# Kernel tuning notes

Measured on AMD Instinct MI355X. Metric: run time of the kernel, lower is better.

## Reference

```python
import jax, jax.numpy as jnp
import numpy as np

N_WIRES = 5
N_OPS = 100000
BATCH = 64
TWO_PI = 6.283185307179586


def _apply_1q(state, U, axis):
    # Apply a shared 2x2 unitary U to the given wire axis of state [B,2,2,2,2,2].
    s = jnp.moveaxis(state, axis, -1)
    s = jnp.einsum('ij,...j->...i', U, s)
    return jnp.moveaxis(s, -1, axis)


def _apply_1q_batched(state, U, axis):
    # Per-batch 2x2 unitaries U: [B,2,2].
    s = jnp.moveaxis(state, axis, -1)
    s = jnp.einsum('bij,b...j->b...i', U, s)
    return jnp.moveaxis(s, -1, axis)


def _rot_unitaries(angles, types):
    # Build [n_ops,2,2] complex64 unitaries: type 0 -> RX, 1 -> RY, 2 -> RZ.
    half = angles * 0.5
    c = jnp.cos(half).astype(jnp.complex64)
    s = jnp.sin(half).astype(jnp.complex64)
    mis = (-1j) * s
    Urx = jnp.stack([jnp.stack([c, mis], -1), jnp.stack([mis, c], -1)], -2)
    Ury = jnp.stack([jnp.stack([c, -s], -1), jnp.stack([s, c], -1)], -2)
    e = jnp.exp((-1j) * half)  # complex64
    zero = jnp.zeros_like(e)
    Urz = jnp.stack([jnp.stack([e, zero], -1), jnp.stack([zero, jnp.conj(e)], -1)], -2)
    t = types[:, None, None]
    return jnp.where(t == 0, Urx, jnp.where(t == 1, Ury, Urz))


def _forward(x, gate_angles, gate_wires, gate_types):
    B = x.shape[0]
    # |00000> initial state per batch item
    state = jnp.zeros((B,) + (2,) * N_WIRES, jnp.complex64)
    state = state.at[(slice(None),) + (0,) * N_WIRES].set(1.0)

    # RxEncoder: RX(x[:, k]) on wire k
    half = x * 0.5
    c = jnp.cos(half).astype(jnp.complex64)
    s = jnp.sin(half).astype(jnp.complex64)
    for k in range(N_WIRES):
        U = jnp.stack([jnp.stack([c[:, k], (-1j) * s[:, k]], -1),
                       jnp.stack([(-1j) * s[:, k], c[:, k]], -1)], -2)  # [B,2,2]
        state = _apply_1q_batched(state, U, k + 1)

    # RandomLayer: long sequential chain of tiny gates on a resident state vector
    Us = _rot_unitaries(gate_angles, gate_types)
    branches = [lambda st, U, a=k + 1: _apply_1q(st, U, a) for k in range(N_WIRES)]

    def step(st, inp):
        U, w = inp
        return jax.lax.switch(w, branches, st, U), None

    state, _ = jax.lax.scan(step, state, (Us, gate_wires))

    # Measure: expval of PauliY on every wire -> [B, 5]
    Y = jnp.array([[0.0, -1j], [1j, 0.0]], jnp.complex64)
    outs = []
    for k in range(N_WIRES):
        ys = _apply_1q(state, Y, k + 1)
        outs.append(jnp.sum(jnp.conj(state) * ys, axis=tuple(range(1, N_WIRES + 1))).real)
    return jnp.stack(outs, -1)


def setup_inputs() -> dict:
    key = jax.random.key(0)
    k1, k2, k3, k4 = jax.random.split(key, 4)
    x = jax.random.normal(k1, (BATCH, N_WIRES), dtype=jnp.float32)
    gate_angles = jax.random.uniform(k2, (N_OPS,), dtype=jnp.float32) * TWO_PI
    gate_wires = jax.random.randint(k3, (N_OPS,), 0, N_WIRES, dtype=jnp.int32)
    gate_types = jax.random.randint(k4, (N_OPS,), 0, 3, dtype=jnp.int32)
    return {"x": x, "gate_angles": gate_angles, "gate_wires": gate_wires, "gate_types": gate_types}


def reference(x, gate_angles, gate_wires, gate_types):
    return _forward(x, gate_angles, gate_wires, gate_types)
```

## Files before the change

### kernel.cpp

```cpp
#include <hip/hip_runtime.h>


#define N_WIRES 5
#define BATCH 64
#define BLOCKS_A 64
#define THREADS_A 256
#define LANES (BLOCKS_A * THREADS_A)
#define QTUP (N_WIRES * 4)

__device__ __forceinline__ void qmul(float* r, const float* b, const float* a) {
    r[0] = b[0]*a[0] - b[1]*a[1] - b[2]*a[2] - b[3]*a[3];
    r[1] = b[0]*a[1] + b[1]*a[0] + b[2]*a[3] - b[3]*a[2];
    r[2] = b[0]*a[2] - b[1]*a[3] + b[2]*a[0] + b[3]*a[1];
    r[3] = b[0]*a[3] + b[1]*a[2] - b[2]*a[1] + b[3]*a[0];
}

__device__ __forceinline__ void wave_reduce6(float* t) {
    for (int st = 1; st < 64; st <<= 1) {
        float o[QTUP];
        #pragma unroll
        for (int i = 0; i < QTUP; ++i) o[i] = __shfl_down(t[i], st, 64);
        #pragma unroll
        for (int w = 0; w < N_WIRES; ++w) {
            float r[4];
            qmul(r, &o[4*w], &t[4*w]);
            t[4*w+0] = r[0]; t[4*w+1] = r[1]; t[4*w+2] = r[2]; t[4*w+3] = r[3];
        }
    }
}

__global__ __launch_bounds__(THREADS_A)
void gate_partials(const float* __restrict__ angles,
                   const int*   __restrict__ wires,
                   const int*   __restrict__ types,
                   int n_ops, int chunk,
                   float* __restrict__ ws)
{
    const int lane = blockIdx.x * THREADS_A + threadIdx.x;

    float acc[N_WIRES][4];
    #pragma unroll
    for (int w = 0; w < N_WIRES; ++w) {
        acc[w][0] = 1.f; acc[w][1] = 0.f; acc[w][2] = 0.f; acc[w][3] = 0.f;
    }

    const int g0 = lane * chunk;
    const int g1 = min(g0 + chunk, n_ops);
    for (int g = g0; g < g1; ++g) {
        const float ang = angles[g];
        const int   w   = wires[g];
        const int   t   = types[g];
        float s, c;
        __sincosf(0.5f * ang, &s, &c);

        float qw = acc[0][0], qx = acc[0][1], qy = acc[0][2], qz = acc[0][3];
        #pragma unroll
        for (int k = 1; k < N_WIRES; ++k) {
            const bool m = (w == k);
            qw = m ? acc[k][0] : qw;  qx = m ? acc[k][1] : qx;
            qy = m ? acc[k][2] : qy;  qz = m ? acc[k][3] : qz;
        }
        const float pw = (t == 0) ? -qx : (t == 1) ? -qy : -qz;
        const float px = (t == 0) ?  qw : (t == 1) ?  qz : -qy;
        const float py = (t == 0) ? -qz : (t == 1) ?  qw :  qx;
        const float pz = (t == 0) ?  qy : (t == 1) ? -qx :  qw;
        const float nw = c*qw + s*pw;
        const float nx = c*qx + s*px;
        const float ny = c*qy + s*py;
        const float nz = c*qz + s*pz;
        #pragma unroll
        for (int k = 0; k < N_WIRES; ++k) {
            const bool m = (w == k);
            acc[k][0] = m ? nw : acc[k][0];  acc[k][1] = m ? nx : acc[k][1];
            acc[k][2] = m ? ny : acc[k][2];  acc[k][3] = m ? nz : acc[k][3];
        }
    }

    float t[QTUP];
    #pragma unroll
    for (int i = 0; i < QTUP; ++i) t[i] = acc[i >> 2][i & 3];
    wave_reduce6(t);

    __shared__ float lds[4][QTUP];
    const int wave = threadIdx.x >> 6;
    if ((threadIdx.x & 63) == 0) {
        #pragma unroll
        for (int i = 0; i < QTUP; ++i) lds[wave][i] = t[i];
    }
    __syncthreads();
    if (threadIdx.x == 0) {
        float r[QTUP];
        #pragma unroll
        for (int i = 0; i < QTUP; ++i) r[i] = lds[0][i];
        #pragma unroll
        for (int v = 1; v < 4; ++v) {
            #pragma unroll
            for (int w = 0; w < N_WIRES; ++w) {
                float z[4];
                qmul(z, &lds[v][4*w], &r[4*w]);
                r[4*w+0] = z[0]; r[4*w+1] = z[1]; r[4*w+2] = z[2]; r[4*w+3] = z[3];
            }
        }
        #pragma unroll
        for (int i = 0; i < QTUP; ++i) ws[blockIdx.x * QTUP + i] = r[i];
    }
}

__global__ __launch_bounds__(320)
void finalize(const float* __restrict__ x,
              const float* __restrict__ ws,
              float* __restrict__ out)
{
    __shared__ float U[QTUP];
    const int tid = threadIdx.x;
    if (tid < 64) {
        float t[QTUP];
        #pragma unroll
        for (int i = 0; i < QTUP; ++i) t[i] = ws[tid * QTUP + i];
        wave_reduce6(t);
        if (tid == 0) {
            #pragma unroll
            for (int i = 0; i < QTUP; ++i) U[i] = t[i];
        }
    }
    __syncthreads();

    if (tid < BATCH * N_WIRES) {
        const int b = tid / N_WIRES;
        const int k = tid % N_WIRES;
        const float xv = x[b * N_WIRES + k];
        float sx, cx;
        __sincosf(0.5f * xv, &sx, &cx);
        const float* q = &U[4*k];
        const float v0r =  cx*q[0] - sx*q[1];
        const float v0i = -cx*q[3] + sx*q[2];
        const float v1r =  cx*q[2] + sx*q[3];
        const float v1i = -cx*q[1] - sx*q[0];
        out[tid] = 2.f * (v0r * v1i - v0i * v1r);
    }
}

extern "C" void kernel_launch(void* const* d_in, const int* in_sizes, int n_in,
                              void* d_out, int out_size, void* d_ws, size_t ws_size,
                              hipStream_t stream) {
    const float* x      = (const float*)d_in[0];
    const float* angles = (const float*)d_in[1];
    const int*   wires  = (const int*)d_in[2];
    const int*   types  = (const int*)d_in[3];
    float* out = (float*)d_out;
    float* ws  = (float*)d_ws;

    const int n_ops = in_sizes[1];
    const int chunk = (n_ops + LANES - 1) / LANES;

    gate_partials<<<BLOCKS_A, THREADS_A, 0, stream>>>(angles, wires, types, n_ops, chunk, ws);
    finalize<<<1, 320, 0, stream>>>(x, ws, out);
}
```

Baseline: 67.37 us.

## Fuse gate reduction and finalize via last-block ticket, vectorize gate loads

Merges the two kernels into one: each block writes its quaternion partial, takes an atomic ticket, and the last block reduces all partials and computes the outputs. Work is spread over 128 blocks with a fixed 4 gates per lane, loaded as float4/int4 with the sincos calls done up front. This removes one kernel launch and the serial per-lane loop, at the cost of an extra memset launch and a fixed CHUNK that only covers n_ops up to 131072 gates.

```diff
diff --git a/kernel.cpp b/kernel.cpp
--- a/kernel.cpp
+++ b/kernel.cpp
@@ -3,10 +3,12 @@
 
 #define N_WIRES 5
 #define BATCH 64
-#define BLOCKS_A 64
-#define THREADS_A 256
-#define LANES (BLOCKS_A * THREADS_A)
+#define NBLK 128
+#define NTHR 256
+#define LANES (NBLK * NTHR)
+#define CHUNK 4
 #define QTUP (N_WIRES * 4)
+#define NWAVE (NTHR / 64)
 
 __device__ __forceinline__ void qmul(float* r, const float* b, const float* a) {
     r[0] = b[0]*a[0] - b[1]*a[1] - b[2]*a[2] - b[3]*a[3];
@@ -29,14 +31,18 @@
     }
 }
 
-__global__ __launch_bounds__(THREADS_A)
-void gate_partials(const float* __restrict__ angles,
+__global__ __launch_bounds__(NTHR)
+void circuit_fused(const float* __restrict__ x,
+                   const float* __restrict__ angles,
                    const int*   __restrict__ wires,
                    const int*   __restrict__ types,
-                   int n_ops, int chunk,
-                   float* __restrict__ ws)
+                   int n_ops,
+                   float* __restrict__ ws,
+                   int*   __restrict__ ticket,
+                   float* __restrict__ out)
 {
-    const int lane = blockIdx.x * THREADS_A + threadIdx.x;
+    const int tid  = threadIdx.x;
+    const int lane = blockIdx.x * NTHR + tid;
 
     float acc[N_WIRES][4];
     #pragma unroll
@@ -44,35 +50,56 @@
         acc[w][0] = 1.f; acc[w][1] = 0.f; acc[w][2] = 0.f; acc[w][3] = 0.f;
     }
 
-    const int g0 = lane * chunk;
-    const int g1 = min(g0 + chunk, n_ops);
-    for (int g = g0; g < g1; ++g) {
-        const float ang = angles[g];
-        const int   w   = wires[g];
-        const int   t   = types[g];
-        float s, c;
-        __sincosf(0.5f * ang, &s, &c);
-
-        float qw = acc[0][0], qx = acc[0][1], qy = acc[0][2], qz = acc[0][3];
+    const int g0 = lane * CHUNK;
+    if (g0 < n_ops) {
+        float ang[CHUNK]; int wv[CHUNK], tv[CHUNK];
+        float sv[CHUNK], cv[CHUNK];
+        if (g0 + CHUNK <= n_ops) {
+            const float4 a4 = *reinterpret_cast<const float4*>(angles + g0);
+            const int4   w4 = *reinterpret_cast<const int4*>(wires + g0);
+            const int4   t4 = *reinterpret_cast<const int4*>(types + g0);
+            ang[0]=a4.x; ang[1]=a4.y; ang[2]=a4.z; ang[3]=a4.w;
+            wv[0]=w4.x;  wv[1]=w4.y;  wv[2]=w4.z;  wv[3]=w4.w;
+            tv[0]=t4.x;  tv[1]=t4.y;  tv[2]=t4.z;  tv[3]=t4.w;
+            #pragma unroll
+            for (int j = 0; j < CHUNK; ++j) __sincosf(0.5f*ang[j], &sv[j], &cv[j]);
+        } else {
+            #pragma unroll
+            for (int j = 0; j < CHUNK; ++j) {
+                const int g = g0 + j;
+                const bool v = (g < n_ops);
+                ang[j] = v ? angles[g] : 0.f;
+                wv[j]  = v ? wires[g]  : 0;
+                tv[j]  = v ? types[g]  : 0;
+                __sincosf(0.5f*ang[j], &sv[j], &cv[j]);
+                if (!v) { sv[j] = 0.f; cv[j] = 1.f; }
+            }
+        }
         #pragma unroll
-        for (int k = 1; k < N_WIRES; ++k) {
-            const bool m = (w == k);
-            qw = m ? acc[k][0] : qw;  qx = m ? acc[k][1] : qx;
-            qy = m ? acc[k][2] : qy;  qz = m ? acc[k][3] : qz;
-        }
-        const float pw = (t == 0) ? -qx : (t == 1) ? -qy : -qz;
-        const float px = (t == 0) ?  qw : (t == 1) ?  qz : -qy;
-        const float py = (t == 0) ? -qz : (t == 1) ?  qw :  qx;
-        const float pz = (t == 0) ?  qy : (t == 1) ? -qx :  qw;
-        const float nw = c*qw + s*pw;
-        const float nx = c*qx + s*px;
-        const float ny = c*qy + s*py;
-        const float nz = c*qz + s*pz;
-        #pragma unroll
-        for (int k = 0; k < N_WIRES; ++k) {
-            const bool m = (w == k);
-            acc[k][0] = m ? nw : acc[k][0];  acc[k][1] = m ? nx : acc[k][1];
-            acc[k][2] = m ? ny : acc[k][2];  acc[k][3] = m ? nz : acc[k][3];
+        for (int j = 0; j < CHUNK; ++j) {
+            const int w = wv[j], t = tv[j];
+            const float s = sv[j], c = cv[j];
+            float qw = acc[0][0], qx = acc[0][1], qy = acc[0][2], qz = acc[0][3];
+            #pragma unroll
+            for (int k = 1; k < N_WIRES; ++k) {
+                const bool m = (w == k);
+                qw = m ? acc[k][0] : qw;  qx = m ? acc[k][1] : qx;
+                qy = m ? acc[k][2] : qy;  qz = m ? acc[k][3] : qz;
+            }
+            const float pw = (t == 0) ? -qx : (t == 1) ? -qy : -qz;
+            const float px = (t == 0) ?  qw : (t == 1) ?  qz : -qy;
+            const float py = (t == 0) ? -qz : (t == 1) ?  qw :  qx;
+            const float pz = (t == 0) ?  qy : (t == 1) ? -qx :  qw;
+            const float nw = c*qw + s*pw;
+            const float nx = c*qx + s*px;
+            const float ny = c*qy + s*py;
+            const float nz = c*qz + s*pz;
+            #pragma unroll
+            for (int k = 0; k < N_WIRES; ++k) {
+                const bool m = (w == k);
+                acc[k][0] = m ? nw : acc[k][0];  acc[k][1] = m ? nx : acc[k][1];
+                acc[k][2] = m ? ny : acc[k][2];  acc[k][3] = m ? nz : acc[k][3];
+            }
         }
     }
 
@@ -81,54 +108,62 @@
     for (int i = 0; i < QTUP; ++i) t[i] = acc[i >> 2][i & 3];
     wave_reduce6(t);
 
-    __shared__ float lds[4][QTUP];
-    const int wave = threadIdx.x >> 6;
-    if ((threadIdx.x & 63) == 0) {
+    __shared__ float lds[NWAVE][QTUP];
+    __shared__ int   is_last;
+    const int wave = tid >> 6;
+    if ((tid & 63) == 0) {
         #pragma unroll
         for (int i = 0; i < QTUP; ++i) lds[wave][i] = t[i];
     }
     __syncthreads();
-    if (threadIdx.x == 0) {
+    if (tid == 0) {
         float r[QTUP];
         #pragma unroll
         for (int i = 0; i < QTUP; ++i) r[i] = lds[0][i];
         #pragma unroll
-        for (int v = 1; v < 4; ++v) {
+        for (int v = 1; v < NWAVE; ++v) {
             #pragma unroll
             for (int w = 0; w < N_WIRES; ++w) {
                 float z[4];
                 qmul(z, &lds[v][4*w], &r[4*w]);
-                r[4*w+0] = z[0]; r[4*w+1] = z[1]; r[4*w+2] = z[2]; r[4*w+3] = z[3];
+                r[4*w+0]=z[0]; r[4*w+1]=z[1]; r[4*w+2]=z[2]; r[4*w+3]=z[3];
             }
         }
         #pragma unroll
         for (int i = 0; i < QTUP; ++i) ws[blockIdx.x * QTUP + i] = r[i];
+        __threadfence();
+        const int tk = atomicAdd(ticket, 1);
+        is_last = (tk == NBLK - 1);
     }
-}
+    __syncthreads();
+    if (!is_last) return;
 
-__global__ __launch_bounds__(320)
-void finalize(const float* __restrict__ x,
-              const float* __restrict__ ws,
-              float* __restrict__ out)
-{
+    __threadfence();
     __shared__ float U[QTUP];
-    const int tid = threadIdx.x;
-    if (tid < 64) {
-        float t[QTUP];
+    float p[QTUP];
+    if (tid < NBLK) {
         #pragma unroll
-        for (int i = 0; i < QTUP; ++i) t[i] = ws[tid * QTUP + i];
-        wave_reduce6(t);
-        if (tid == 0) {
+        for (int i = 0; i < QTUP; ++i) p[i] = ws[tid * QTUP + i];
+        wave_reduce6(p);
+        if ((tid & 63) == 0) {
             #pragma unroll
-            for (int i = 0; i < QTUP; ++i) U[i] = t[i];
+            for (int i = 0; i < QTUP; ++i) lds[tid >> 6][i] = p[i];
+        }
+    }
+    __syncthreads();
+    if (tid == 0) {
+        #pragma unroll
+        for (int w = 0; w < N_WIRES; ++w) {
+            float z[4];
+            qmul(z, &lds[1][4*w], &lds[0][4*w]);
+            U[4*w+0]=z[0]; U[4*w+1]=z[1]; U[4*w+2]=z[2]; U[4*w+3]=z[3];
         }
     }
     __syncthreads();
 
-    if (tid < BATCH * N_WIRES) {
-        const int b = tid / N_WIRES;
-        const int k = tid % N_WIRES;
-        const float xv = x[b * N_WIRES + k];
+    for (int o = tid; o < BATCH * N_WIRES; o += NTHR) {
+        const int k = o % N_WIRES;
+        const float xv = x[o];
         float sx, cx;
         __sincosf(0.5f * xv, &sx, &cx);
         const float* q = &U[4*k];
@@ -136,7 +171,7 @@
         const float v0i = -cx*q[3] + sx*q[2];
         const float v1r =  cx*q[2] + sx*q[3];
         const float v1i = -cx*q[1] - sx*q[0];
-        out[tid] = 2.f * (v0r * v1i - v0i * v1r);
+        out[o] = 2.f * (v0r * v1i - v0i * v1r);
     }
 }
 
@@ -149,10 +184,11 @@
     const int*   types  = (const int*)d_in[3];
     float* out = (float*)d_out;
     float* ws  = (float*)d_ws;
+    int* ticket = (int*)((char*)d_ws + NBLK * QTUP * sizeof(float));
 
     const int n_ops = in_sizes[1];
-    const int chunk = (n_ops + LANES - 1) / LANES;
 
-    gate_partials<<<BLOCKS_A, THREADS_A, 0, stream>>>(angles, wires, types, n_ops, chunk, ws);
-    finalize<<<1, 320, 0, stream>>>(x, ws, out);
+    hipMemsetAsync(ticket, 0, sizeof(int), stream);
+    circuit_fused<<<NBLK, NTHR, 0, stream>>>(x, angles, wires, types, n_ops,
+                                             ws, ticket, out);
 }
```

New measurement: 69.93 us. +3.8%, slower.
